# Performance work log

Hardware: AMD Instinct MI355X
Metric: run time of the kernel (lower is better)

## Reference

```python
import jax, jax.numpy as jnp
import numpy as np
from jax import lax

B, CIN, COUT, H, W = 4, 256, 256, 64, 64
K = 3  # kernel size
PAD = 1
STRIDE = 1


def setup_inputs() -> dict:
    key = jax.random.key(0)
    k1, k2, k3, k4 = jax.random.split(key, 4)
    x = jax.random.normal(k1, (B, CIN, H, W), dtype=jnp.float32)
    # small offset weights so learned offsets are modest (original init is zeros)
    offset_w = jax.random.normal(k2, (3 * K * K, CIN, K, K), dtype=jnp.float32) * 0.01
    offset_b = jax.random.normal(k3, (3 * K * K,), dtype=jnp.float32) * 0.01
    dcn_w = jax.random.normal(k4, (COUT, CIN, K, K), dtype=jnp.float32) * (1.0 / np.sqrt(CIN * K * K))
    return {"x": x, "offset_w": offset_w, "offset_b": offset_b, "dcn_w": dcn_w}


def _dcnv2(x, offset_w, offset_b, dcn_w):
    b, c, h, w = x.shape
    kk = K * K
    # offset conv (standard 3x3, stride 1, pad 1)
    o = lax.conv_general_dilated(
        x, offset_w, (STRIDE, STRIDE), ((PAD, PAD), (PAD, PAD)),
        dimension_numbers=("NCHW", "OIHW", "NCHW"))
    o = o + offset_b[None, :, None, None]
    ho, wo = o.shape[2], o.shape[3]
    off = o[:, : 2 * kk].reshape(b, kk, 2, ho, wo)  # pairs are (dy, dx)
    dy, dx = off[:, :, 0], off[:, :, 1]             # [b,kk,ho,wo]
    mask = jax.nn.sigmoid(o[:, 2 * kk:])            # [b,kk,ho,wo]

    ki, kj = jnp.meshgrid(jnp.arange(K), jnp.arange(K), indexing="ij")
    ki = ki.reshape(kk).astype(jnp.float32)
    kj = kj.reshape(kk).astype(jnp.float32)
    base_y = (jnp.arange(ho, dtype=jnp.float32) * STRIDE - PAD)[None, None, :, None] + ki[None, :, None, None]
    base_x = (jnp.arange(wo, dtype=jnp.float32) * STRIDE - PAD)[None, None, None, :] + kj[None, :, None, None]
    py = base_y + dy  # [b,kk,ho,wo] sampling y
    px = base_x + dx  # sampling x

    y0 = jnp.floor(py)
    x0 = jnp.floor(px)
    wy = py - y0  # bilinear fractional weights
    wx = px - x0
    y0i = y0.astype(jnp.int32)
    x0i = x0.astype(jnp.int32)

    xT = x.transpose(0, 2, 3, 1)  # [b,h,w,c] for channel-last gathers
    bidx = jnp.arange(b)[:, None, None, None]

    def gather(yi, xi):
        # zero padding outside the image
        valid = (yi >= 0) & (yi < h) & (xi >= 0) & (xi < w)
        yc = jnp.clip(yi, 0, h - 1)
        xc = jnp.clip(xi, 0, w - 1)
        v = xT[bidx, yc, xc]  # [b,kk,ho,wo,c]
        return v * valid[..., None].astype(x.dtype)

    g00 = gather(y0i, x0i)
    g01 = gather(y0i, x0i + 1)
    g10 = gather(y0i + 1, x0i)
    g11 = gather(y0i + 1, x0i + 1)

    wy_ = wy[..., None]
    wx_ = wx[..., None]
    sampled = (g00 * (1 - wy_) * (1 - wx_) + g01 * (1 - wy_) * wx_
               + g10 * wy_ * (1 - wx_) + g11 * wy_ * wx_)
    sampled = sampled * mask[..., None]  # modulation

    wk = dcn_w.reshape(dcn_w.shape[0], c, kk)  # [o,c,kk]
    return jnp.einsum("bkhwc,ock->bohw", sampled, wk)


def reference(x, offset_w, offset_b, dcn_w):
    return _dcnv2(x, offset_w, offset_b, dcn_w)
```

## Files before the change

kernel.cpp:

```cpp
#include <hip/hip_runtime.h>
#include <hip/hip_bf16.h>
#include <stdint.h>
#include <math.h>

#define KDIM 2304
#define PS   1296
#define PB   10368

typedef __attribute__((ext_vector_type(8))) short bf16x8;
typedef __attribute__((ext_vector_type(8))) unsigned short u16x8;
typedef __attribute__((ext_vector_type(4))) float f32x4;

__device__ inline unsigned short f2bf(float f) {
  union { float f; unsigned int u; } v; v.f = f;
  unsigned int u = v.u;
  unsigned int r = (u + 0x7FFFu + ((u >> 16) & 1u)) >> 16;
  return (unsigned short)r;
}
__device__ inline float bf2f(unsigned short h) {
  union { unsigned int u; float f; } v; v.u = ((unsigned int)h) << 16;
  return v.f;
}

__global__ __launch_bounds__(256) void k_transpose(const float* __restrict__ x,
                                                   unsigned short* __restrict__ xTb) {
  __shared__ float tile[32][33];
  int t = threadIdx.x;
  int tx = t & 31, ty = t >> 5;
  int p0 = blockIdx.x * 32;
  int c0 = blockIdx.y * 32;
  int b  = blockIdx.z;
  const float* xb = x + ((size_t)b << 20);
#pragma unroll
  for (int i = 0; i < 4; ++i) {
    int c = c0 + ty + i * 8;
    tile[ty + i * 8][tx] = xb[((size_t)c << 12) + p0 + tx];
  }
  __syncthreads();
  unsigned short* ob = xTb + ((size_t)b << 20);
#pragma unroll
  for (int i = 0; i < 4; ++i) {
    int p = p0 + ty + i * 8;
    ob[(((size_t)p) << 8) + c0 + tx] = f2bf(tile[tx][ty + i * 8]);
  }
}

__global__ __launch_bounds__(256) void k_wprep(const float* __restrict__ dcn_w,
                                               const float* __restrict__ offset_w,
                                               unsigned short* __restrict__ Wpk,
                                               unsigned short* __restrict__ Wob,
                                               unsigned short* __restrict__ zp) {
  int gid = blockIdx.x * 256 + threadIdx.x;
  const int N1 = 72 * 8192;
  const int N2 = 32 * KDIM;
  if (gid < N1) {
    int j = gid & 7;
    int lane = (gid >> 3) & 63;
    int mb = (gid >> 9) & 15;
    int kc = gid >> 13;
    int row = mb * 16 + (lane & 15);
    int gk = kc * 32 + ((lane >> 4) << 3) + j;
    int c = gk & 255, kidx = gk >> 8;
    Wpk[gid] = f2bf(dcn_w[((size_t)(row * 256 + c)) * 9 + kidx]);
  } else if (gid < N1 + N2) {
    int g = gid - N1;
    int ch = g / KDIM, k = g % KDIM;
    int kidx = k >> 8, c = k & 255;
    Wob[g] = (ch < 27) ? f2bf(offset_w[((size_t)(ch * 256 + c)) * 9 + kidx])
                       : (unsigned short)0;
  } else if (gid < N1 + N2 + 256) {
    zp[gid - N1 - N2] = 0;
  }
}

__global__ __launch_bounds__(256, 2) void k_offs_gemm(const unsigned short* __restrict__ xTb,
                                                      const unsigned short* __restrict__ Wob,
                                                      const unsigned short* __restrict__ zp,
                                                      float* __restrict__ O2) {
  __shared__ __align__(16) unsigned short As[2 * PB];
  int t = threadIdx.x;
  int wv = t >> 6, lane = t & 63;
  int cl = lane & 15, q = lane >> 4;
  int wm = wv & 1, wn = wv >> 1;
  int n0 = blockIdx.x * 32;

  int r = t >> 3, kc = t & 7;
  int row = n0 + r;
  int b_ = row >> 12, hw = row & 4095, h = hw >> 6, w = hw & 63;
  const unsigned short* xbb = xTb + ((size_t)b_ << 20);

  f32x4 acc = {};

  auto stage = [&](int p, int bufsel) {
    int di = p / 3 - 1, dj = p % 3 - 1;
    int y = h + di, xx = w + dj;
    bool v = ((unsigned)y < 64u) && ((unsigned)xx < 64u);
    const unsigned short* src = v ? xbb + (((size_t)((y << 6) + xx)) << 8) + kc * 32
                                  : zp;
    unsigned short* dst = As + bufsel * PB + kc * PS + r * 40;
#pragma unroll
    for (int si = 0; si < 4; ++si)
      *(u16x8*)(dst + si * 8) = *(const u16x8*)(src + si * 8);
  };

  auto mmphase = [&](int p, int bufsel) {
    const unsigned short* base = As + bufsel * PB;
#pragma unroll
    for (int k2 = 0; k2 < 8; ++k2) {
      int kt = p * 8 + k2;
      bf16x8 aF = *(const bf16x8*)(base + k2 * PS + (wm * 16 + cl) * 40 + q * 8);
      bf16x8 bF = *(const bf16x8*)(Wob + (size_t)(wn * 16 + cl) * KDIM + kt * 32 + q * 8);
      acc = __builtin_amdgcn_mfma_f32_16x16x32_bf16(aF, bF, acc, 0, 0, 0);
    }
  };

  stage(0, 0);
  __syncthreads();
#pragma unroll 1
  for (int p = 0; p < 9; ++p) {
    if (p < 8) stage(p + 1, (p + 1) & 1);
    mmphase(p, p & 1);
    __syncthreads();
  }

#pragma unroll
  for (int rr = 0; rr < 4; ++rr)
    O2[(size_t)(n0 + wm * 16 + q * 4 + rr) * 32 + wn * 16 + cl] = acc[rr];
}

__global__ __launch_bounds__(256) void k_sweights(const float* __restrict__ O2,
                                                  const float* __restrict__ offb,
                                                  float* __restrict__ SW) {
  int gid = blockIdx.x * 256 + threadIdx.x;
  if (gid >= 9 * 16384) return;
  int k = gid >> 14;
  int bhw = gid & 16383;
  int h = (bhw >> 6) & 63, w = bhw & 63;

  const float* o = O2 + (size_t)bhw * 32;
  float dy = o[2 * k]     + offb[2 * k];
  float dx = o[2 * k + 1] + offb[2 * k + 1];
  float mv = o[18 + k]    + offb[18 + k];
  float mask = 1.0f / (1.0f + expf(-mv));

  float py = (float)(h - 1 + k / 3) + dy;
  float px = (float)(w - 1 + k % 3) + dx;
  float y0f = floorf(py), x0f = floorf(px);
  float wy = py - y0f, wx = px - x0f;
  int y0 = (int)y0f, x0 = (int)x0f;
  int y1 = y0 + 1, x1 = x0 + 1;

  float vy0 = (y0 >= 0 && y0 < 64) ? 1.f : 0.f;
  float vy1 = (y1 >= 0 && y1 < 64) ? 1.f : 0.f;
  float vx0 = (x0 >= 0 && x0 < 64) ? 1.f : 0.f;
  float vx1 = (x1 >= 0 && x1 < 64) ? 1.f : 0.f;
  int y0c = min(max(y0, 0), 63), y1c = min(max(y1, 0), 63);
  int x0c = min(max(x0, 0), 63), x1c = min(max(x1, 0), 63);

  float4 wv4;
  wv4.x = (1.f - wy) * (1.f - wx) * vy0 * vx0 * mask;
  wv4.y = (1.f - wy) * wx * vy0 * vx1 * mask;
  wv4.z = wy * (1.f - wx) * vy1 * vx0 * mask;
  wv4.w = wy * wx * vy1 * vx1 * mask;
  uint4 ov;
  ov.x = (unsigned)(((y0c << 6) + x0c) << 8);
  ov.y = (unsigned)(((y0c << 6) + x1c) << 8);
  ov.z = (unsigned)(((y1c << 6) + x0c) << 8);
  ov.w = (unsigned)(((y1c << 6) + x1c) << 8);

  float* p = SW + (size_t)gid * 8;
  *(float4*)p = wv4;
  *(uint4*)(p + 4) = ov;
}

__global__ __launch_bounds__(256, 2) void k_fused(const unsigned short* __restrict__ Wpk,
                                                  const unsigned short* __restrict__ xTb,
                                                  const float* __restrict__ SW,
                                                  float* __restrict__ out) {
  __shared__ __align__(16) unsigned short Bs[2 * PB];
  int t = threadIdx.x;
  int wv = t >> 6, lane = t & 63;
  int cl = lane & 15, q = lane >> 4;
  int n0 = blockIdx.x * 32;
  int b  = n0 >> 12;
  const unsigned short* xb = xTb + ((size_t)b << 20);

  int r = t >> 3, kc = t & 7;

  f32x4 acc[4][2] = {};

  auto sample = [&](int p, int bufsel) {
    const float* sw = SW + ((size_t)((p << 14) + n0 + r)) * 8;
    float4 wq = *(const float4*)sw;
    uint4 ov = *(const uint4*)(sw + 4);
    int co = kc * 32;
    const unsigned short* p00 = xb + ov.x + co;
    const unsigned short* p01 = xb + ov.y + co;
    const unsigned short* p10 = xb + ov.z + co;
    const unsigned short* p11 = xb + ov.w + co;
    u16x8 ca[4], cb[4], cc[4], cd[4];
#pragma unroll
    for (int si = 0; si < 4; ++si) {
      ca[si] = *(const u16x8*)(p00 + si * 8);
      cb[si] = *(const u16x8*)(p01 + si * 8);
      cc[si] = *(const u16x8*)(p10 + si * 8);
      cd[si] = *(const u16x8*)(p11 + si * 8);
    }
    unsigned short* dst = Bs + bufsel * PB + kc * PS + r * 40;
#pragma unroll
    for (int si = 0; si < 4; ++si) {
      float s[8];
#pragma unroll
      for (int c2 = 0; c2 < 8; ++c2)
        s[c2] = wq.x * bf2f(ca[si][c2]) + wq.y * bf2f(cb[si][c2])
              + wq.z * bf2f(cc[si][c2]) + wq.w * bf2f(cd[si][c2]);
      union { __hip_bfloat162 h2[4]; u16x8 v; } pk;
#pragma unroll
      for (int c2 = 0; c2 < 4; ++c2)
        pk.h2[c2] = __float22bfloat162_rn(make_float2(s[2 * c2], s[2 * c2 + 1]));
      *(u16x8*)(dst + si * 8) = pk.v;
    }
  };

  auto mmphase = [&](int p, int bufsel) {
    const unsigned short* base = Bs + bufsel * PB;
    bf16x8 aF[4], aFn[4];
#pragma unroll
    for (int i = 0; i < 4; ++i)
      aF[i] = *(const bf16x8*)(Wpk + ((size_t)((p * 8 * 16 + wv * 4 + i) * 64 + lane)) * 8);
#pragma unroll
    for (int k2 = 0; k2 < 8; ++k2) {
      if (k2 < 7) {
        int kt = p * 8 + k2 + 1;
#pragma unroll
        for (int i = 0; i < 4; ++i)
          aFn[i] = *(const bf16x8*)(Wpk + ((size_t)((kt * 16 + wv * 4 + i) * 64 + lane)) * 8);
      }
      bf16x8 bF[2];
#pragma unroll
      for (int j = 0; j < 2; ++j)
        bF[j] = *(const bf16x8*)(base + k2 * PS + (j * 16 + cl) * 40 + q * 8);
#pragma unroll
      for (int i = 0; i < 4; ++i) {
        acc[i][0] = __builtin_amdgcn_mfma_f32_16x16x32_bf16(aF[i], bF[0], acc[i][0], 0, 0, 0);
        acc[i][1] = __builtin_amdgcn_mfma_f32_16x16x32_bf16(aF[i], bF[1], acc[i][1], 0, 0, 0);
      }
      if (k2 < 7) {
#pragma unroll
        for (int i = 0; i < 4; ++i) aF[i] = aFn[i];
      }
    }
  };

  sample(0, 0);
  __syncthreads();
#pragma unroll 1
  for (int p = 0; p < 9; ++p) {
    if (p < 8) sample(p + 1, (p + 1) & 1);
    mmphase(p, p & 1);
    __syncthreads();
  }

  float* ob = out + (((size_t)b) << 20);
  int hwb = n0 & 4095;
#pragma unroll
  for (int i = 0; i < 4; ++i) {
    int mbase = wv * 64 + i * 16 + q * 4;
#pragma unroll
    for (int j = 0; j < 2; ++j) {
      float* op = ob + hwb + j * 16 + cl;
#pragma unroll
      for (int rr = 0; rr < 4; ++rr)
        op[((size_t)(mbase + rr)) << 12] = acc[i][j][rr];
    }
  }
}

extern "C" void kernel_launch(void* const* d_in, const int* in_sizes, int n_in,
                              void* d_out, int out_size, void* d_ws, size_t ws_size,
                              hipStream_t stream) {
  const float* x        = (const float*)d_in[0];
  const float* offset_w = (const float*)d_in[1];
  const float* offset_b = (const float*)d_in[2];
  const float* dcn_w    = (const float*)d_in[3];
  float* out = (float*)d_out;

  char* ws = (char*)d_ws;
  size_t off = 0;
  auto carve = [&](size_t bytes) -> void* {
    void* p = ws + off;
    off += (bytes + 255) & ~(size_t)255;
    return p;
  };
  unsigned short* xTb = (unsigned short*)carve(4ull * 64 * 64 * 256 * 2);
  unsigned short* Wpk = (unsigned short*)carve(72ull * 8192 * 2);
  unsigned short* Wob = (unsigned short*)carve(32ull * KDIM * 2);
  unsigned short* zp  = (unsigned short*)carve(512);
  float*          O2  = (float*)carve(16384ull * 32 * 4);
  float*          SW  = (float*)carve(9ull * 16384 * 8 * 4);
  (void)ws_size; (void)in_sizes; (void)n_in; (void)out_size;

  k_transpose<<<dim3(128, 8, 4), 256, 0, stream>>>(x, xTb);
  k_wprep<<<dim3((72 * 8192 + 32 * KDIM + 256 + 255) / 256), 256, 0, stream>>>(
      dcn_w, offset_w, Wpk, Wob, zp);
  k_offs_gemm<<<dim3(512), 256, 0, stream>>>(xTb, Wob, zp, O2);
  k_sweights<<<dim3((9 * 16384 + 255) / 256), 256, 0, stream>>>(O2, offset_b, SW);
  k_fused<<<dim3(512), 256, 0, stream>>>(Wpk, xTb, SW, out);
}
```

Baseline: 164.2 us.

## Prefetch gathers into registers with single LDS buffer; enlarge fused tile to 64 pixels

Both GEMM kernels now prefetch the next tap's global gathers into registers, then write them to a single LDS buffer after the MFMA phase, replacing the double-buffered LDS staging. Staging threads are remapped so each thread handles one 8-element channel chunk across several rows, which gives more coalesced gather loads. The fused kernel moves to 512-thread blocks covering 64 pixels with a 4x2 wave split over output channels and pixels, so each weight fragment is reused across more pixels. It also prefetches the sampling weights two taps ahead. The cost is extra register pressure from the prefetched gathers and half as many blocks (256) on the GPU.

Result: no change. 166.4 us (+1.3%).

```diff
diff --git a/kernel.cpp b/kernel.cpp
--- a/kernel.cpp
+++ b/kernel.cpp
@@ -4,8 +4,8 @@
 #include <math.h>
 
 #define KDIM 2304
-#define PS   1296
-#define PB   10368
+#define PSF  2576
+#define PSO  1296
 
 typedef __attribute__((ext_vector_type(8))) short bf16x8;
 typedef __attribute__((ext_vector_type(8))) unsigned short u16x8;
@@ -68,7 +68,7 @@
     int kidx = k >> 8, c = k & 255;
     Wob[g] = (ch < 27) ? f2bf(offset_w[((size_t)(ch * 256 + c)) * 9 + kidx])
                        : (unsigned short)0;
-  } else if (gid < N1 + N2 + 256) {
+  } else if (gid < N1 + N2 + 512) {
     zp[gid - N1 - N2] = 0;
   }
 }
@@ -77,55 +77,62 @@
                                                       const unsigned short* __restrict__ Wob,
                                                       const unsigned short* __restrict__ zp,
                                                       float* __restrict__ O2) {
-  __shared__ __align__(16) unsigned short As[2 * PB];
+  __shared__ __align__(16) unsigned short As[8 * PSO];
   int t = threadIdx.x;
   int wv = t >> 6, lane = t & 63;
   int cl = lane & 15, q = lane >> 4;
   int wm = wv & 1, wn = wv >> 1;
   int n0 = blockIdx.x * 32;
 
-  int r = t >> 3, kc = t & 7;
-  int row = n0 + r;
-  int b_ = row >> 12, hw = row & 4095, h = hw >> 6, w = hw & 63;
-  const unsigned short* xbb = xTb + ((size_t)b_ << 20);
+  int rowb = t >> 5;
+  int s = t & 31;
+  int kcp = s >> 2, soff = (s & 3) * 8, sE = s * 8;
+
+  int hh[4], ww[4];
+  const unsigned short* xbb[4];
+#pragma unroll
+  for (int i = 0; i < 4; ++i) {
+    int row = n0 + rowb + 8 * i;
+    int b_ = row >> 12, hw = row & 4095;
+    hh[i] = hw >> 6; ww[i] = hw & 63;
+    xbb[i] = xTb + ((size_t)b_ << 20);
+  }
+
+  auto gsrc = [&](int p, int i) -> const unsigned short* {
+    int di = p / 3 - 1, dj = p % 3 - 1;
+    int y = hh[i] + di, xx = ww[i] + dj;
+    bool v = ((unsigned)y < 64u) && ((unsigned)xx < 64u);
+    return v ? xbb[i] + (((size_t)((y << 6) + xx)) << 8) + sE : zp + sE;
+  };
 
   f32x4 acc = {};
-
-  auto stage = [&](int p, int bufsel) {
-    int di = p / 3 - 1, dj = p % 3 - 1;
-    int y = h + di, xx = w + dj;
-    bool v = ((unsigned)y < 64u) && ((unsigned)xx < 64u);
-    const unsigned short* src = v ? xbb + (((size_t)((y << 6) + xx)) << 8) + kc * 32
-                                  : zp;
-    unsigned short* dst = As + bufsel * PB + kc * PS + r * 40;
-#pragma unroll
-    for (int si = 0; si < 4; ++si)
-      *(u16x8*)(dst + si * 8) = *(const u16x8*)(src + si * 8);
-  };
-
-  auto mmphase = [&](int p, int bufsel) {
-    const unsigned short* base = As + bufsel * PB;
+  u16x8 g[4];
+#pragma unroll
+  for (int i = 0; i < 4; ++i) g[i] = *(const u16x8*)gsrc(0, i);
+
+#pragma unroll 1
+  for (int p = 0; p < 9; ++p) {
+#pragma unroll
+    for (int i = 0; i < 4; ++i)
+      *(u16x8*)(&As[kcp * PSO + (rowb + 8 * i) * 40 + soff]) = g[i];
+    if (p < 8) {
+#pragma unroll
+      for (int i = 0; i < 4; ++i) g[i] = *(const u16x8*)gsrc(p + 1, i);
+    }
+    __syncthreads();
 #pragma unroll
     for (int k2 = 0; k2 < 8; ++k2) {
       int kt = p * 8 + k2;
-      bf16x8 aF = *(const bf16x8*)(base + k2 * PS + (wm * 16 + cl) * 40 + q * 8);
+      bf16x8 aF = *(const bf16x8*)(&As[k2 * PSO + (wm * 16 + cl) * 40 + q * 8]);
       bf16x8 bF = *(const bf16x8*)(Wob + (size_t)(wn * 16 + cl) * KDIM + kt * 32 + q * 8);
       acc = __builtin_amdgcn_mfma_f32_16x16x32_bf16(aF, bF, acc, 0, 0, 0);
     }
-  };
-
-  stage(0, 0);
-  __syncthreads();
-#pragma unroll 1
-  for (int p = 0; p < 9; ++p) {
-    if (p < 8) stage(p + 1, (p + 1) & 1);
-    mmphase(p, p & 1);
     __syncthreads();
   }
 
 #pragma unroll
-  for (int rr = 0; rr < 4; ++rr)
-    O2[(size_t)(n0 + wm * 16 + q * 4 + rr) * 32 + wn * 16 + cl] = acc[rr];
+  for (int r = 0; r < 4; ++r)
+    O2[(size_t)(n0 + wm * 16 + q * 4 + r) * 32 + wn * 16 + cl] = acc[r];
 }
 
 __global__ __launch_bounds__(256) void k_sweights(const float* __restrict__ O2,
@@ -173,91 +180,103 @@
   *(uint4*)(p + 4) = ov;
 }
 
-__global__ __launch_bounds__(256, 2) void k_fused(const unsigned short* __restrict__ Wpk,
+__global__ __launch_bounds__(512, 2) void k_fused(const unsigned short* __restrict__ Wpk,
                                                   const unsigned short* __restrict__ xTb,
                                                   const float* __restrict__ SW,
                                                   float* __restrict__ out) {
-  __shared__ __align__(16) unsigned short Bs[2 * PB];
+  __shared__ __align__(16) unsigned short Bs[8 * PSF];
   int t = threadIdx.x;
   int wv = t >> 6, lane = t & 63;
+  int wm = wv & 3, wn = wv >> 2;
   int cl = lane & 15, q = lane >> 4;
-  int n0 = blockIdx.x * 32;
+  int n0 = blockIdx.x * 64;
   int b  = n0 >> 12;
   const unsigned short* xb = xTb + ((size_t)b << 20);
 
-  int r = t >> 3, kc = t & 7;
+  int rowb = t >> 5;
+  int s = t & 31;
+  int kcp = s >> 2, soff = (s & 3) * 8, sE = s * 8;
 
   f32x4 acc[4][2] = {};
-
-  auto sample = [&](int p, int bufsel) {
-    const float* sw = SW + ((size_t)((p << 14) + n0 + r)) * 8;
-    float4 wq = *(const float4*)sw;
-    uint4 ov = *(const uint4*)(sw + 4);
-    int co = kc * 32;
-    const unsigned short* p00 = xb + ov.x + co;
-    const unsigned short* p01 = xb + ov.y + co;
-    const unsigned short* p10 = xb + ov.z + co;
-    const unsigned short* p11 = xb + ov.w + co;
-    u16x8 ca[4], cb[4], cc[4], cd[4];
-#pragma unroll
-    for (int si = 0; si < 4; ++si) {
-      ca[si] = *(const u16x8*)(p00 + si * 8);
-      cb[si] = *(const u16x8*)(p01 + si * 8);
-      cc[si] = *(const u16x8*)(p10 + si * 8);
-      cd[si] = *(const u16x8*)(p11 + si * 8);
-    }
-    unsigned short* dst = Bs + bufsel * PB + kc * PS + r * 40;
-#pragma unroll
-    for (int si = 0; si < 4; ++si) {
-      float s[8];
-#pragma unroll
-      for (int c2 = 0; c2 < 8; ++c2)
-        s[c2] = wq.x * bf2f(ca[si][c2]) + wq.y * bf2f(cb[si][c2])
-              + wq.z * bf2f(cc[si][c2]) + wq.w * bf2f(cd[si][c2]);
-      union { __hip_bfloat162 h2[4]; u16x8 v; } pk;
-#pragma unroll
-      for (int c2 = 0; c2 < 4; ++c2)
-        pk.h2[c2] = __float22bfloat162_rn(make_float2(s[2 * c2], s[2 * c2 + 1]));
-      *(u16x8*)(dst + si * 8) = pk.v;
-    }
-  };
-
-  auto mmphase = [&](int p, int bufsel) {
-    const unsigned short* base = Bs + bufsel * PB;
-    bf16x8 aF[4], aFn[4];
-#pragma unroll
-    for (int i = 0; i < 4; ++i)
-      aF[i] = *(const bf16x8*)(Wpk + ((size_t)((p * 8 * 16 + wv * 4 + i) * 64 + lane)) * 8);
-#pragma unroll
-    for (int k2 = 0; k2 < 8; ++k2) {
-      if (k2 < 7) {
-        int kt = p * 8 + k2 + 1;
-#pragma unroll
-        for (int i = 0; i < 4; ++i)
-          aFn[i] = *(const bf16x8*)(Wpk + ((size_t)((kt * 16 + wv * 4 + i) * 64 + lane)) * 8);
-      }
-      bf16x8 bF[2];
-#pragma unroll
-      for (int j = 0; j < 2; ++j)
-        bF[j] = *(const bf16x8*)(base + k2 * PS + (j * 16 + cl) * 40 + q * 8);
-#pragma unroll
-      for (int i = 0; i < 4; ++i) {
-        acc[i][0] = __builtin_amdgcn_mfma_f32_16x16x32_bf16(aF[i], bF[0], acc[i][0], 0, 0, 0);
-        acc[i][1] = __builtin_amdgcn_mfma_f32_16x16x32_bf16(aF[i], bF[1], acc[i][1], 0, 0, 0);
-      }
-      if (k2 < 7) {
-#pragma unroll
-        for (int i = 0; i < 4; ++i) aF[i] = aFn[i];
-      }
-    }
-  };
-
-  sample(0, 0);
-  __syncthreads();
+  float4 wqs[4], wqc[4];
+  uint4  ovc[4];
+  u16x8 g0[4], g1[4], g2[4], g3[4];
+  bf16x8 aC[4], aN[4];
+
+#pragma unroll
+  for (int i = 0; i < 4; ++i) {
+    const float* sw = SW + ((size_t)(n0 + rowb + 16 * i)) * 8;
+    wqc[i] = *(const float4*)sw; ovc[i] = *(const uint4*)(sw + 4);
+  }
+#pragma unroll
+  for (int i = 0; i < 4; ++i) {
+    g0[i] = *(const u16x8*)(xb + ovc[i].x + sE);
+    g1[i] = *(const u16x8*)(xb + ovc[i].y + sE);
+    g2[i] = *(const u16x8*)(xb + ovc[i].z + sE);
+    g3[i] = *(const u16x8*)(xb + ovc[i].w + sE);
+    wqs[i] = wqc[i];
+  }
+#pragma unroll
+  for (int i = 0; i < 4; ++i) {
+    const float* sw = SW + ((size_t)((1 << 14) + n0 + rowb + 16 * i)) * 8;
+    wqc[i] = *(const float4*)sw; ovc[i] = *(const uint4*)(sw + 4);
+  }
+#pragma unroll
+  for (int i = 0; i < 4; ++i)
+    aC[i] = *(const bf16x8*)(Wpk + ((size_t)((wm * 4 + i) * 64 + lane)) * 8);
+
 #pragma unroll 1
   for (int p = 0; p < 9; ++p) {
-    if (p < 8) sample(p + 1, (p + 1) & 1);
-    mmphase(p, p & 1);
+#pragma unroll
+    for (int i = 0; i < 4; ++i) {
+      float sv[8];
+#pragma unroll
+      for (int c = 0; c < 8; ++c)
+        sv[c] = wqs[i].x * bf2f(g0[i][c]) + wqs[i].y * bf2f(g1[i][c])
+              + wqs[i].z * bf2f(g2[i][c]) + wqs[i].w * bf2f(g3[i][c]);
+      union { __hip_bfloat162 h2[4]; u16x8 v; } pk;
+#pragma unroll
+      for (int c = 0; c < 4; ++c)
+        pk.h2[c] = __float22bfloat162_rn(make_float2(sv[2 * c], sv[2 * c + 1]));
+      *(u16x8*)(&Bs[kcp * PSF + (rowb + 16 * i) * 40 + soff]) = pk.v;
+    }
+    if (p < 8) {
+#pragma unroll
+      for (int i = 0; i < 4; ++i) {
+        g0[i] = *(const u16x8*)(xb + ovc[i].x + sE);
+        g1[i] = *(const u16x8*)(xb + ovc[i].y + sE);
+        g2[i] = *(const u16x8*)(xb + ovc[i].z + sE);
+        g3[i] = *(const u16x8*)(xb + ovc[i].w + sE);
+        wqs[i] = wqc[i];
+      }
+    }
+    __syncthreads();
+    if (p < 7) {
+#pragma unroll
+      for (int i = 0; i < 4; ++i) {
+        const float* sw = SW + ((size_t)(((p + 2) << 14) + n0 + rowb + 16 * i)) * 8;
+        wqc[i] = *(const float4*)sw; ovc[i] = *(const uint4*)(sw + 4);
+      }
+    }
+#pragma unroll
+    for (int k2 = 0; k2 < 8; ++k2) {
+      int kt = p * 8 + k2;
+      int ktn = (kt + 1 < 72) ? kt + 1 : kt;
+#pragma unroll
+      for (int i = 0; i < 4; ++i)
+        aN[i] = *(const bf16x8*)(Wpk + ((size_t)((ktn * 16 + wm * 4 + i) * 64 + lane)) * 8);
+      bf16x8 bF[2];
+#pragma unroll
+      for (int j = 0; j < 2; ++j)
+        bF[j] = *(const bf16x8*)(&Bs[k2 * PSF + (wn * 32 + j * 16 + cl) * 40 + q * 8]);
+#pragma unroll
+      for (int i = 0; i < 4; ++i) {
+        acc[i][0] = __builtin_amdgcn_mfma_f32_16x16x32_bf16(aC[i], bF[0], acc[i][0], 0, 0, 0);
+        acc[i][1] = __builtin_amdgcn_mfma_f32_16x16x32_bf16(aC[i], bF[1], acc[i][1], 0, 0, 0);
+      }
+#pragma unroll
+      for (int i = 0; i < 4; ++i) aC[i] = aN[i];
+    }
     __syncthreads();
   }
 
@@ -265,10 +284,10 @@
   int hwb = n0 & 4095;
 #pragma unroll
   for (int i = 0; i < 4; ++i) {
-    int mbase = wv * 64 + i * 16 + q * 4;
+    int mbase = wm * 64 + i * 16 + q * 4;
 #pragma unroll
     for (int j = 0; j < 2; ++j) {
-      float* op = ob + hwb + j * 16 + cl;
+      float* op = ob + hwb + wn * 32 + j * 16 + cl;
 #pragma unroll
       for (int rr = 0; rr < 4; ++rr)
         op[((size_t)(mbase + rr)) << 12] = acc[i][j][rr];
@@ -295,15 +314,15 @@
   unsigned short* xTb = (unsigned short*)carve(4ull * 64 * 64 * 256 * 2);
   unsigned short* Wpk = (unsigned short*)carve(72ull * 8192 * 2);
   unsigned short* Wob = (unsigned short*)carve(32ull * KDIM * 2);
-  unsigned short* zp  = (unsigned short*)carve(512);
+  unsigned short* zp  = (unsigned short*)carve(1024);
   float*          O2  = (float*)carve(16384ull * 32 * 4);
   float*          SW  = (float*)carve(9ull * 16384 * 8 * 4);
   (void)ws_size; (void)in_sizes; (void)n_in; (void)out_size;
 
   k_transpose<<<dim3(128, 8, 4), 256, 0, stream>>>(x, xTb);
-  k_wprep<<<dim3((72 * 8192 + 32 * KDIM + 256 + 255) / 256), 256, 0, stream>>>(
+  k_wprep<<<dim3((72 * 8192 + 32 * KDIM + 512 + 255) / 256), 256, 0, stream>>>(
       dcn_w, offset_w, Wpk, Wob, zp);
   k_offs_gemm<<<dim3(512), 256, 0, stream>>>(xTb, Wob, zp, O2);
   k_sweights<<<dim3((9 * 16384 + 255) / 256), 256, 0, stream>>>(O2, offset_b, SW);
-  k_fused<<<dim3(512), 256, 0, stream>>>(Wpk, xTb, SW, out);
-}
+  k_fused<<<dim3(256), 512, 0, stream>>>(Wpk, xTb, SW, out);
+}
```
